# Kernel tuning notes

Hardware: AMD Instinct MI355X
Metric: run time of the kernel (lower is better)

## Reference

```python
import jax, jax.numpy as jnp
import numpy as np
from jax import lax

B, CIN, H, W = 16, 256, 64, 64
DP = 512          # displace_planes
COUT = 256        # outplanes
NUM_OFFSET = 64   # displace_planes // BIND_CHAN(8)
K = 5             # DPOOL_SIZE (odd)
EPS = float(np.finfo(np.float32).eps)
BN_EPS = 1e-5
EXP_CLAMP = 88.722835


def conv1x1(x, w, b):
    # x: [B,C,H,W], w: [O,C], b: [O]
    return jnp.einsum('bchw,oc->bohw', x, w) + b[None, :, None, None]


def batchnorm(x, gamma, beta):
    m = x.mean(axis=(0, 2, 3))
    v = x.var(axis=(0, 2, 3))
    inv = lax.rsqrt(v + BN_EPS)
    return (x - m[None, :, None, None]) * (inv * gamma)[None, :, None, None] + beta[None, :, None, None]


def dynamic_pool(x, sigma):
    # per-channel Gaussian depthwise conv in exp space, back to log space
    r = (jnp.arange(K) - K // 2).astype(jnp.float32)
    dissq = r[:, None] ** 2 + r[None, :] ** 2                     # [K,K]
    kern = jnp.exp(-(dissq / 2.0)[None] / (sigma ** 2 + EPS)[:, None, None])  # [C,K,K]
    kern = kern / kern.sum(axis=(1, 2), keepdims=True)
    expx = jnp.exp(jnp.minimum(x, EXP_CLAMP))
    out = lax.conv_general_dilated(
        expx, kern[:, None],                                      # rhs [C,1,K,K]
        window_strides=(1, 1), padding=[(K // 2, K // 2)] * 2,
        dimension_numbers=('NCHW', 'OIHW', 'NCHW'),
        feature_group_count=DP)
    return jnp.log(out + EPS)


def displace(feat, offsets):
    # feat: [B,C,H,W]; offsets: [NUM_OFFSET,2] (dy,dx), each bound to C//NUM_OFFSET channels.
    # Per-channel uniform bilinear shift with zero padding outside the map.
    Bn, C, Hn, Wn = feat.shape
    chan = C // NUM_OFFSET
    dy = jnp.repeat(offsets[:, 0], chan)  # [C]
    dx = jnp.repeat(offsets[:, 1], chan)
    y0 = jnp.floor(dy); x0 = jnp.floor(dx)
    fy = dy - y0; fx = dx - x0            # fractional parts (diff. wrt offsets)
    y0i = y0.astype(jnp.int32); x0i = x0.astype(jnp.int32)
    rows = jnp.arange(Hn); cols = jnp.arange(Wn)

    def one_chan(img, y0c, x0c, fyc, fxc):
        # img: [B,H,W]; shift is separable per row/col since offset is uniform
        def shifted(oy, ox):
            ry = rows + y0c + oy
            rx = cols + x0c + ox
            my = (ry >= 0) & (ry < Hn)
            mx = (rx >= 0) & (rx < Wn)
            g = img[:, jnp.clip(ry, 0, Hn - 1), :][:, :, jnp.clip(rx, 0, Wn - 1)]
            return g * (my[:, None] & mx[None, :]).astype(img.dtype)[None]
        return ((1 - fyc) * (1 - fxc) * shifted(0, 0)
                + (1 - fyc) * fxc * shifted(0, 1)
                + fyc * (1 - fxc) * shifted(1, 0)
                + fyc * fxc * shifted(1, 1))

    return jax.vmap(one_chan, in_axes=(1, 0, 0, 0, 0), out_axes=1)(feat, y0i, x0i, fy, fx)


def attention(x, w, b, gamma, beta):
    a = conv1x1(x, w, b)
    a = batchnorm(a, gamma, beta)
    a = jax.nn.softplus(a)
    # SpaceNormalization: normalize over spatial dims
    return a / a.sum(axis=(2, 3), keepdims=True)


def setup_inputs() -> dict:
    key = jax.random.key(0)
    ks = jax.random.split(key, 6)
    return {
        'x': jax.random.normal(ks[0], (B, CIN, H, W), jnp.float32),
        'pre_w': jax.random.normal(ks[1], (DP, CIN), jnp.float32) / np.sqrt(CIN),
        'pre_b': jnp.zeros((DP,), jnp.float32),
        'sigma': jnp.full((DP,), K / 2 / 2, jnp.float32),
        'offsets': jax.random.normal(ks[2], (NUM_OFFSET, 2), jnp.float32) * 3.0,
        'atten_w': jax.random.normal(ks[3], (DP, CIN), jnp.float32) / np.sqrt(CIN),
        'atten_b': jnp.zeros((DP,), jnp.float32),
        'atten_gamma': jnp.ones((DP,), jnp.float32),
        'atten_beta': jnp.zeros((DP,), jnp.float32),
        'post_w': jax.random.normal(ks[4], (COUT, DP), jnp.float32) / np.sqrt(DP),
        'post_b': jnp.zeros((COUT,), jnp.float32),
        'bn_gamma': jnp.ones((COUT,), jnp.float32),
        'bn_beta': jnp.zeros((COUT,), jnp.float32),
    }


def reference(x, pre_w, pre_b, sigma, offsets, atten_w, atten_b, atten_gamma,
              atten_beta, post_w, post_b, bn_gamma, bn_beta):
    out_pre = conv1x1(x, pre_w, pre_b)                 # [B,DP,H,W]
    out_pre = dynamic_pool(out_pre, sigma)
    out_dis = displace(out_pre, offsets)
    out_atten = attention(x, atten_w, atten_b, atten_gamma, atten_beta)
    out_post = conv1x1(out_atten * out_dis, post_w, post_b)  # [B,COUT,H,W]
    out_skip = x + out_post                            # inplanes==outplanes, stride=1
    return jax.nn.relu(batchnorm(out_skip, bn_gamma, bn_beta))
```

## Files before the change

kernel.cpp:

```cpp
#include <hip/hip_runtime.h>
#include <cmath>

#define NB   16
#define CINC 256
#define DPC  512
#define COUTC 256
#define HWS  4096
#define EPSF 1.1920928955078125e-07f
#define BN_EPS 1e-5f
#define EXP_CLAMP 88.722835f
#define TS 76
#define PS 72

typedef unsigned int uint32;
typedef unsigned short ushort;
typedef __bf16 bf16x8 __attribute__((ext_vector_type(8)));
typedef float f32x4 __attribute__((ext_vector_type(4)));
typedef unsigned short ushort8 __attribute__((ext_vector_type(8)));

__device__ inline ushort f2bf(float f) {
    __bf16 h = (__bf16)f;
    return __builtin_bit_cast(ushort, h);
}
__device__ inline float bf2f(ushort u) {
    return __builtin_bit_cast(float, (uint32)u << 16);
}
__device__ inline float softplus_fast(float v) {
    return fmaxf(v, 0.f) + __logf(1.f + __expf(-fabsf(v)));
}
__device__ __forceinline__ void gload16(const void* g, void* l) {
    __builtin_amdgcn_global_load_lds(
        (__attribute__((address_space(1))) void*)g,
        (__attribute__((address_space(3))) void*)l, 16, 0, 0);
}

template<int OTOT, int KTOT, bool BF16_OUT, bool ADD_SKIP>
__global__ __launch_bounds__(256) void mfma_gemm_k(
    const ushort* __restrict__ A, const ushort* __restrict__ BT,
    const float* __restrict__ bias1, const float* __restrict__ bias2,
    const float* __restrict__ skip, void* __restrict__ outv) {
    const int hw0 = blockIdx.x * 128;
    const int o0  = blockIdx.y * 128;
    const int b   = blockIdx.z;
    __shared__ ushort As[2 * 128 * 32];
    __shared__ ushort Bs[2 * 128 * 32];
    const int tid  = threadIdx.x;
    const int lane = tid & 63;
    const int w    = tid >> 6;
    const int wm0  = (w >> 1) * 64;
    const int wn0  = (w & 1) * 64;

    f32x4 acc[4][4] = {};

    const ushort* Ab = A + (size_t)o0 * KTOT;
    const ushort* Bb = BT + ((size_t)b * HWS + hw0) * KTOT;
    const int rsub  = lane >> 2;
    const int ksubp = ((lane & 3) ^ ((lane >> 3) & 3)) * 8;

    for (int step = 0; step < KTOT / 64; ++step) {
        const int k0 = step * 64;
#pragma unroll
        for (int h = 0; h < 2; ++h)
#pragma unroll
            for (int i = 0; i < 2; ++i) {
                const int row = w * 32 + i * 16 + rsub;
                gload16(Ab + (size_t)row * KTOT + k0 + h * 32 + ksubp,
                        &As[h * 4096 + (w * 32 + i * 16) * 32]);
                gload16(Bb + (size_t)row * KTOT + k0 + h * 32 + ksubp,
                        &Bs[h * 4096 + (w * 32 + i * 16) * 32]);
            }
        __syncthreads();
        bf16x8 af[2][4], bfr[2][4];
#pragma unroll
        for (int h = 0; h < 2; ++h) {
#pragma unroll
            for (int mi = 0; mi < 4; ++mi) {
                int row = wm0 + mi * 16 + (lane & 15);
                int sl = (lane >> 4) ^ ((row >> 1) & 3);
                af[h][mi] = *reinterpret_cast<const bf16x8*>(As + h * 4096 + row * 32 + sl * 8);
            }
#pragma unroll
            for (int ni = 0; ni < 4; ++ni) {
                int row = wn0 + ni * 16 + (lane & 15);
                int sl = (lane >> 4) ^ ((row >> 1) & 3);
                bfr[h][ni] = *reinterpret_cast<const bf16x8*>(Bs + h * 4096 + row * 32 + sl * 8);
            }
        }
#pragma unroll
        for (int h = 0; h < 2; ++h)
#pragma unroll
            for (int mi = 0; mi < 4; ++mi)
#pragma unroll
                for (int ni = 0; ni < 4; ++ni)
                    acc[mi][ni] = __builtin_amdgcn_mfma_f32_16x16x32_bf16(
                        af[h][mi], bfr[h][ni], acc[mi][ni], 0, 0, 0);
        __syncthreads();
    }

#pragma unroll
    for (int mi = 0; mi < 4; ++mi) {
#pragma unroll
        for (int r = 0; r < 4; ++r) {
            int o = o0 + wm0 + mi * 16 + ((lane >> 4) << 2) + r;
            float bi = (o < 512) ? bias1[o] : bias2[o - 512];
            size_t base = ((size_t)b * OTOT + o) * HWS + hw0 + wn0 + (lane & 15);
            if constexpr (BF16_OUT) {
                ushort* outp = (ushort*)outv;
#pragma unroll
                for (int ni = 0; ni < 4; ++ni)
                    outp[base + ni * 16] = f2bf(acc[mi][ni][r] + bi);
            } else {
                float* outp = (float*)outv;
#pragma unroll
                for (int ni = 0; ni < 4; ++ni) {
                    float v = acc[mi][ni][r] + bi;
                    if constexpr (ADD_SKIP) v += skip[base + ni * 16];
                    outp[base + ni * 16] = v;
                }
            }
        }
    }
}

__global__ __launch_bounds__(256) void castT_k(const float* __restrict__ x,
                                               ushort* __restrict__ xT) {
    const int b = blockIdx.z, c0 = blockIdx.y * 64, hw0 = blockIdx.x * 64;
    __shared__ float tile[64][65];
    const int tid = threadIdx.x;
#pragma unroll
    for (int r = 0; r < 16; ++r) {
        int cl = r * 4 + (tid >> 6), hwl = tid & 63;
        tile[cl][hwl] = x[((size_t)b * CINC + c0 + cl) * HWS + hw0 + hwl];
    }
    __syncthreads();
#pragma unroll
    for (int r = 0; r < 16; ++r) {
        int hwl = r * 4 + (tid >> 6), cl = tid & 63;
        xT[((size_t)b * HWS + hw0 + hwl) * CINC + c0 + cl] = f2bf(tile[cl][hwl]);
    }
}

__global__ __launch_bounds__(256) void cast_k(const float* __restrict__ in,
                                              ushort* __restrict__ out, int n) {
    int i = (blockIdx.x * 256 + threadIdx.x) * 4;
    if (i < n) {
        float4 v = *reinterpret_cast<const float4*>(in + i);
        out[i + 0] = f2bf(v.x); out[i + 1] = f2bf(v.y);
        out[i + 2] = f2bf(v.z); out[i + 3] = f2bf(v.w);
    }
}

__global__ __launch_bounds__(256) void pooldisp_k(ushort* __restrict__ dp,
                                                  const float* __restrict__ sigma,
                                                  const float* __restrict__ offsets) {
    const int bc = blockIdx.x;
    const int b = bc >> 9, c = bc & 511;
    __shared__ float  tmp[68 * TS];
    __shared__ ushort pl[64 * PS];
    const int tid = threadIdx.x;
    ushort* ip = dp + ((size_t)b * 1024 + c) * HWS;

    float s = sigma[c];
    float inv = 0.5f / (s * s + EPSF);
    float g0 = __expf(-4.f * inv), g1 = __expf(-1.f * inv);
    float gs = g0 + g1 + 1.f + g1 + g0;
    float rnorm = 1.f / (gs * gs);

    if (tid < 64) {
        int r = tid >> 4;
        int rr = (r < 2) ? r : 64 + r;
        int cq = (tid & 15) * 4;
        f32x4 z = {0.f, 0.f, 0.f, 0.f};
        *reinterpret_cast<f32x4*>(&tmp[rr * TS + cq]) = z;
    }
#pragma unroll
    for (int t = 0; t < 2; ++t) {
        int task = tid + t * 256;
        int hr = task >> 3, w0 = (task & 7) * 8;
        const ushort* rp = ip + hr * 64 + w0;
        ushort8 mv = *reinterpret_cast<const ushort8*>(rp);
        float e[12];
        e[0] = (w0 > 0) ? __expf(fminf(bf2f(rp[-2]), EXP_CLAMP)) : 0.f;
        e[1] = (w0 > 0) ? __expf(fminf(bf2f(rp[-1]), EXP_CLAMP)) : 0.f;
#pragma unroll
        for (int q = 0; q < 8; ++q)
            e[2 + q] = __expf(fminf(bf2f(mv[q]), EXP_CLAMP));
        e[10] = (w0 < 56) ? __expf(fminf(bf2f(rp[8]), EXP_CLAMP)) : 0.f;
        e[11] = (w0 < 56) ? __expf(fminf(bf2f(rp[9]), EXP_CLAMP)) : 0.f;
        f32x4 o0, o1;
#pragma unroll
        for (int j = 0; j < 4; ++j) {
            o0[j] = g0 * (e[j] + e[j + 4]) + g1 * (e[j + 1] + e[j + 3]) + e[j + 2];
            o1[j] = g0 * (e[j + 4] + e[j + 8]) + g1 * (e[j + 5] + e[j + 7]) + e[j + 6];
        }
        *reinterpret_cast<f32x4*>(&tmp[(hr + 2) * TS + w0]) = o0;
        *reinterpret_cast<f32x4*>(&tmp[(hr + 2) * TS + w0 + 4]) = o1;
    }
    __syncthreads();

#pragma unroll
    for (int t = 0; t < 4; ++t) {
        int task = tid + t * 256;
        int h = task >> 4, wq = (task & 15) * 4;
        f32x4 t0 = *reinterpret_cast<const f32x4*>(&tmp[(h + 0) * TS + wq]);
        f32x4 t1 = *reinterpret_cast<const f32x4*>(&tmp[(h + 1) * TS + wq]);
        f32x4 t2 = *reinterpret_cast<const f32x4*>(&tmp[(h + 2) * TS + wq]);
        f32x4 t3 = *reinterpret_cast<const f32x4*>(&tmp[(h + 3) * TS + wq]);
        f32x4 t4 = *reinterpret_cast<const f32x4*>(&tmp[(h + 4) * TS + wq]);
        ushort o[4];
#pragma unroll
        for (int j = 0; j < 4; ++j) {
            float v = g0 * (t0[j] + t4[j]) + g1 * (t1[j] + t3[j]) + t2[j];
            o[j] = f2bf(__logf(v * rnorm + EPSF));
        }
        *reinterpret_cast<uint32*>(&pl[h * PS + wq]) =
            (uint32)o[0] | ((uint32)o[1] << 16);
        *reinterpret_cast<uint32*>(&pl[h * PS + wq + 2]) =
            (uint32)o[2] | ((uint32)o[3] << 16);
    }
    __syncthreads();

    int oi = c >> 3;
    float dy = offsets[oi * 2 + 0];
    float dx = offsets[oi * 2 + 1];
    float y0f = floorf(dy), x0f = floorf(dx);
    float fy = dy - y0f, fx = dx - x0f;
    int y0 = (int)y0f, x0 = (int)x0f;
    float w00 = (1.f - fy) * (1.f - fx), w01 = (1.f - fy) * fx;
    float w10 = fy * (1.f - fx),         w11 = fy * fx;
#pragma unroll
    for (int t = 0; t < 2; ++t) {
        int p = (tid + t * 256) * 8;
        int h = p >> 6, w = p & 63;
        int ry0 = h + y0, ry1 = ry0 + 1;
        bool my0 = (ry0 >= 0) & (ry0 < 64);
        bool my1 = (ry1 >= 0) & (ry1 < 64);
        ushort8 ov;
#pragma unroll
        for (int q = 0; q < 8; ++q) {
            int rx0 = w + q + x0, rx1 = rx0 + 1;
            bool mx0 = (rx0 >= 0) & (rx0 < 64);
            bool mx1 = (rx1 >= 0) & (rx1 < 64);
            float acc = 0.f;
            if (my0 & mx0) acc += w00 * bf2f(pl[ry0 * PS + rx0]);
            if (my0 & mx1) acc += w01 * bf2f(pl[ry0 * PS + rx1]);
            if (my1 & mx0) acc += w10 * bf2f(pl[ry1 * PS + rx0]);
            if (my1 & mx1) acc += w11 * bf2f(pl[ry1 * PS + rx1]);
            ov[q] = f2bf(acc);
        }
        *reinterpret_cast<ushort8*>(ip + p) = ov;
    }
}

__global__ __launch_bounds__(1024) void attstats_k(const ushort* __restrict__ dp,
                                                   const float* __restrict__ gamma,
                                                   const float* __restrict__ beta,
                                                   float* __restrict__ scale,
                                                   float* __restrict__ shift,
                                                   float* __restrict__ rsum) {
    const int c = blockIdx.x;
    const int t = threadIdx.x;
    const int wv = t >> 6, lane = t & 63;
    const ushort* p = dp + ((size_t)wv * 1024 + 512 + c) * HWS;

    ushort8 v[8];
    float s = 0.f, s2 = 0.f;
#pragma unroll
    for (int k = 0; k < 8; ++k) {
        v[k] = *reinterpret_cast<const ushort8*>(p + lane * 8 + k * 512);
#pragma unroll
        for (int j = 0; j < 8; ++j) { float f = bf2f(v[k][j]); s += f; s2 += f * f; }
    }
#pragma unroll
    for (int off = 32; off > 0; off >>= 1) {
        s += __shfl_down(s, off, 64);
        s2 += __shfl_down(s2, off, 64);
    }
    __shared__ float t1[16], t2[16], scsh[2];
    if (lane == 0) { t1[wv] = s; t2[wv] = s2; }
    __syncthreads();
    if (t == 0) {
        float S = 0.f, S2 = 0.f;
#pragma unroll
        for (int k = 0; k < 16; ++k) { S += t1[k]; S2 += t2[k]; }
        float n = (float)(NB * HWS);
        float mean = S / n;
        float var = S2 / n - mean * mean;
        float invs = rsqrtf(var + BN_EPS);
        float sc = invs * gamma[c];
        float sh = beta[c] - mean * sc;
        scale[c] = sc; shift[c] = sh;
        scsh[0] = sc; scsh[1] = sh;
    }
    __syncthreads();
    float sc = scsh[0], sh = scsh[1];
    float ps = 0.f;
#pragma unroll
    for (int k = 0; k < 8; ++k)
#pragma unroll
        for (int j = 0; j < 8; ++j)
            ps += softplus_fast(bf2f(v[k][j]) * sc + sh);
#pragma unroll
    for (int off = 32; off > 0; off >>= 1) ps += __shfl_down(ps, off, 64);
    if (lane == 0) rsum[wv * DPC + c] = 1.f / ps;
}

__global__ __launch_bounds__(256) void attmulT_k(const ushort* __restrict__ dp,
                                                 const float* __restrict__ scale,
                                                 const float* __restrict__ shift,
                                                 const float* __restrict__ rsum,
                                                 ushort* __restrict__ mT) {
    const int b = blockIdx.z, c0 = blockIdx.y * 64, hw0 = blockIdx.x * 64;
    __shared__ float tile[64][65];
    const int tid = threadIdx.x;
#pragma unroll
    for (int r = 0; r < 16; ++r) {
        int cl = r * 4 + (tid >> 6), hwl = tid & 63;
        int c = c0 + cl;
        size_t aidx = ((size_t)b * 1024 + 512 + c) * HWS + hw0 + hwl;
        size_t didx = ((size_t)b * 1024 + c) * HWS + hw0 + hwl;
        float a = bf2f(dp[aidx]) * scale[c] + shift[c];
        float m = softplus_fast(a) * rsum[b * DPC + c] * bf2f(dp[didx]);
        tile[cl][hwl] = m;
    }
    __syncthreads();
#pragma unroll
    for (int r = 0; r < 16; ++r) {
        int hwl = r * 4 + (tid >> 6), cl = tid & 63;
        mT[((size_t)b * HWS + hw0 + hwl) * DPC + c0 + cl] = f2bf(tile[cl][hwl]);
    }
}

__global__ __launch_bounds__(1024) void bnstats_k(const float* __restrict__ a,
                                                  const float* __restrict__ gamma,
                                                  const float* __restrict__ beta,
                                                  float* __restrict__ scale,
                                                  float* __restrict__ shift) {
    const int c = blockIdx.x;
    const int t = threadIdx.x;
    const int wv = t >> 6, lane = t & 63;
    const float* p = a + ((size_t)wv * COUTC + c) * HWS;
    float s = 0.f, s2 = 0.f;
#pragma unroll
    for (int k = 0; k < 16; ++k) {
        float4 v = *reinterpret_cast<const float4*>(p + lane * 4 + k * 256);
        s += v.x + v.y + v.z + v.w;
        s2 += v.x * v.x + v.y * v.y + v.z * v.z + v.w * v.w;
    }
#pragma unroll
    for (int off = 32; off > 0; off >>= 1) {
        s += __shfl_down(s, off, 64);
        s2 += __shfl_down(s2, off, 64);
    }
    __shared__ float t1[16], t2[16];
    if (lane == 0) { t1[wv] = s; t2[wv] = s2; }
    __syncthreads();
    if (t == 0) {
        float S = 0.f, S2 = 0.f;
#pragma unroll
        for (int k = 0; k < 16; ++k) { S += t1[k]; S2 += t2[k]; }
        float n = (float)(NB * HWS);
        float mean = S / n;
        float var = S2 / n - mean * mean;
        float invs = rsqrtf(var + BN_EPS);
        float sc = invs * gamma[c];
        scale[c] = sc;
        shift[c] = beta[c] - mean * sc;
    }
}

__global__ __launch_bounds__(256) void final_k(float* __restrict__ out,
                                               const float* __restrict__ scale,
                                               const float* __restrict__ shift) {
    int i = blockIdx.x * 256 + threadIdx.x;
    int c = (i >> 12) & (COUTC - 1);
    float v = out[i] * scale[c] + shift[c];
    out[i] = fmaxf(v, 0.f);
}

extern "C" void kernel_launch(void* const* d_in, const int* in_sizes, int n_in,
                              void* d_out, int out_size, void* d_ws, size_t ws_size,
                              hipStream_t stream) {
    const float* x           = (const float*)d_in[0];
    const float* pre_w       = (const float*)d_in[1];
    const float* pre_b       = (const float*)d_in[2];
    const float* sigma       = (const float*)d_in[3];
    const float* offsets     = (const float*)d_in[4];
    const float* atten_w     = (const float*)d_in[5];
    const float* atten_b     = (const float*)d_in[6];
    const float* atten_gamma = (const float*)d_in[7];
    const float* atten_beta  = (const float*)d_in[8];
    const float* post_w      = (const float*)d_in[9];
    const float* post_b      = (const float*)d_in[10];
    const float* bn_gamma    = (const float*)d_in[11];
    const float* bn_beta     = (const float*)d_in[12];
    float* out = (float*)d_out;

    char* wsb = (char*)d_ws;
    ushort* xT    = (ushort*)(wsb);
    ushort* wbig  = (ushort*)(wsb + ((size_t)32 << 20));
    ushort* wpost = wbig + 1024 * 256;
    float*  stats = (float*)(wsb + ((size_t)33 << 20));
    ushort* dpout = (ushort*)(wsb + ((size_t)34 << 20));
    ushort* mT    = (ushort*)(wsb + ((size_t)162 << 20));

    float* scaleA = stats;
    float* shiftA = stats + 512;
    float* rsum   = stats + 1024;
    float* scale2 = stats + 9216;
    float* shift2 = stats + 9472;

    castT_k<<<dim3(64, 4, NB), 256, 0, stream>>>(x, xT);
    cast_k<<<128, 256, 0, stream>>>(pre_w,   wbig,             DPC * CINC);
    cast_k<<<128, 256, 0, stream>>>(atten_w, wbig + 512 * 256, DPC * CINC);
    cast_k<<<128, 256, 0, stream>>>(post_w,  wpost,            COUTC * DPC);

    mfma_gemm_k<1024, CINC, true, false><<<dim3(32, 8, NB), 256, 0, stream>>>(
        wbig, xT, pre_b, atten_b, nullptr, dpout);
    pooldisp_k<<<NB * DPC, 256, 0, stream>>>(dpout, sigma, offsets);
    attstats_k<<<DPC, 1024, 0, stream>>>(dpout, atten_gamma, atten_beta,
                                         scaleA, shiftA, rsum);
    attmulT_k<<<dim3(64, 8, NB), 256, 0, stream>>>(dpout, scaleA, shiftA, rsum, mT);
    mfma_gemm_k<COUTC, DPC, false, true><<<dim3(32, 2, NB), 256, 0, stream>>>(
        wpost, mT, post_b, post_b, x, out);
    bnstats_k<<<COUTC, 1024, 0, stream>>>(out, bn_gamma, bn_beta, scale2, shift2);
    final_k<<<out_size / 256, 256, 0, stream>>>(out, scale2, shift2);
}
```

Baseline: 297.9 us.

## Widen pool/displace blocks to 512 threads and reuse shifted row samples

The fused pool+displace kernel now runs with 512 threads per block and one task per thread instead of looping, with launch bounds asking for higher occupancy. The bilinear displacement loads 9 samples per row once into registers and reuses them across the 8 outputs, replacing 32 guarded LDS reads with 18. The plane LDS stride is changed to 66 to alter bank mapping. This may raise register pressure under the tighter launch bounds.

```diff
diff --git a/kernel.cpp b/kernel.cpp
--- a/kernel.cpp
+++ b/kernel.cpp
@@ -10,7 +10,7 @@
 #define BN_EPS 1e-5f
 #define EXP_CLAMP 88.722835f
 #define TS 76
-#define PS 72
+#define PS2 66
 
 typedef unsigned int uint32;
 typedef unsigned short ushort;
@@ -150,13 +150,13 @@
     }
 }
 
-__global__ __launch_bounds__(256) void pooldisp_k(ushort* __restrict__ dp,
-                                                  const float* __restrict__ sigma,
-                                                  const float* __restrict__ offsets) {
+__global__ __launch_bounds__(512, 8) void pooldisp_k(ushort* __restrict__ dp,
+                                                     const float* __restrict__ sigma,
+                                                     const float* __restrict__ offsets) {
     const int bc = blockIdx.x;
     const int b = bc >> 9, c = bc & 511;
     __shared__ float  tmp[68 * TS];
-    __shared__ ushort pl[64 * PS];
+    __shared__ ushort pl[64 * PS2];
     const int tid = threadIdx.x;
     ushort* ip = dp + ((size_t)b * 1024 + c) * HWS;
 
@@ -166,17 +166,15 @@
     float gs = g0 + g1 + 1.f + g1 + g0;
     float rnorm = 1.f / (gs * gs);
 
-    if (tid < 64) {
-        int r = tid >> 4;
-        int rr = (r < 2) ? r : 64 + r;
-        int cq = (tid & 15) * 4;
-        f32x4 z = {0.f, 0.f, 0.f, 0.f};
-        *reinterpret_cast<f32x4*>(&tmp[rr * TS + cq]) = z;
-    }
-#pragma unroll
-    for (int t = 0; t < 2; ++t) {
-        int task = tid + t * 256;
-        int hr = task >> 3, w0 = (task & 7) * 8;
+    {
+        int r4 = tid >> 7, col = tid & 127;
+        if (col < TS) {
+            int row = (r4 < 2) ? r4 : 64 + r4;
+            tmp[row * TS + col] = 0.f;
+        }
+    }
+    {
+        int hr = tid >> 3, w0 = (tid & 7) * 8;
         const ushort* rp = ip + hr * 64 + w0;
         ushort8 mv = *reinterpret_cast<const ushort8*>(rp);
         float e[12];
@@ -199,8 +197,8 @@
     __syncthreads();
 
 #pragma unroll
-    for (int t = 0; t < 4; ++t) {
-        int task = tid + t * 256;
+    for (int t = 0; t < 2; ++t) {
+        int task = tid + t * 512;
         int h = task >> 4, wq = (task & 15) * 4;
         f32x4 t0 = *reinterpret_cast<const f32x4*>(&tmp[(h + 0) * TS + wq]);
         f32x4 t1 = *reinterpret_cast<const f32x4*>(&tmp[(h + 1) * TS + wq]);
@@ -213,42 +211,40 @@
             float v = g0 * (t0[j] + t4[j]) + g1 * (t1[j] + t3[j]) + t2[j];
             o[j] = f2bf(__logf(v * rnorm + EPSF));
         }
-        *reinterpret_cast<uint32*>(&pl[h * PS + wq]) =
+        *reinterpret_cast<uint32*>(&pl[h * PS2 + wq]) =
             (uint32)o[0] | ((uint32)o[1] << 16);
-        *reinterpret_cast<uint32*>(&pl[h * PS + wq + 2]) =
+        *reinterpret_cast<uint32*>(&pl[h * PS2 + wq + 2]) =
             (uint32)o[2] | ((uint32)o[3] << 16);
     }
     __syncthreads();
 
-    int oi = c >> 3;
-    float dy = offsets[oi * 2 + 0];
-    float dx = offsets[oi * 2 + 1];
-    float y0f = floorf(dy), x0f = floorf(dx);
-    float fy = dy - y0f, fx = dx - x0f;
-    int y0 = (int)y0f, x0 = (int)x0f;
-    float w00 = (1.f - fy) * (1.f - fx), w01 = (1.f - fy) * fx;
-    float w10 = fy * (1.f - fx),         w11 = fy * fx;
-#pragma unroll
-    for (int t = 0; t < 2; ++t) {
-        int p = (tid + t * 256) * 8;
-        int h = p >> 6, w = p & 63;
+    {
+        int oi = c >> 3;
+        float dy = offsets[oi * 2 + 0];
+        float dx = offsets[oi * 2 + 1];
+        float y0f = floorf(dy), x0f = floorf(dx);
+        float fy = dy - y0f, fx = dx - x0f;
+        int y0 = (int)y0f, x0 = (int)x0f;
+        float w00 = (1.f - fy) * (1.f - fx), w01 = (1.f - fy) * fx;
+        float w10 = fy * (1.f - fx),         w11 = fy * fx;
+        int h = tid >> 3, w = (tid & 7) * 8;
         int ry0 = h + y0, ry1 = ry0 + 1;
         bool my0 = (ry0 >= 0) & (ry0 < 64);
         bool my1 = (ry1 >= 0) & (ry1 < 64);
+        float e0[9], e1[9];
+#pragma unroll
+        for (int j = 0; j < 9; ++j) {
+            int col = w + x0 + j;
+            bool mx = (col >= 0) & (col < 64);
+            e0[j] = (my0 & mx) ? bf2f(pl[ry0 * PS2 + col]) : 0.f;
+            e1[j] = (my1 & mx) ? bf2f(pl[ry1 * PS2 + col]) : 0.f;
+        }
         ushort8 ov;
 #pragma unroll
-        for (int q = 0; q < 8; ++q) {
-            int rx0 = w + q + x0, rx1 = rx0 + 1;
-            bool mx0 = (rx0 >= 0) & (rx0 < 64);
-            bool mx1 = (rx1 >= 0) & (rx1 < 64);
-            float acc = 0.f;
-            if (my0 & mx0) acc += w00 * bf2f(pl[ry0 * PS + rx0]);
-            if (my0 & mx1) acc += w01 * bf2f(pl[ry0 * PS + rx1]);
-            if (my1 & mx0) acc += w10 * bf2f(pl[ry1 * PS + rx0]);
-            if (my1 & mx1) acc += w11 * bf2f(pl[ry1 * PS + rx1]);
-            ov[q] = f2bf(acc);
-        }
-        *reinterpret_cast<ushort8*>(ip + p) = ov;
+        for (int q = 0; q < 8; ++q)
+            ov[q] = f2bf(w00 * e0[q] + w01 * e0[q + 1]
+                       + w10 * e1[q] + w11 * e1[q + 1]);
+        *reinterpret_cast<ushort8*>(ip + tid * 8) = ov;
     }
 }
 
@@ -417,7 +413,7 @@
 
     mfma_gemm_k<1024, CINC, true, false><<<dim3(32, 8, NB), 256, 0, stream>>>(
         wbig, xT, pre_b, atten_b, nullptr, dpout);
-    pooldisp_k<<<NB * DPC, 256, 0, stream>>>(dpout, sigma, offsets);
+    pooldisp_k<<<NB * DPC, 512, 0, stream>>>(dpout, sigma, offsets);
     attstats_k<<<DPC, 1024, 0, stream>>>(dpout, atten_gamma, atten_beta,
                                          scaleA, shiftA, rsum);
     attmulT_k<<<dim3(64, 8, NB), 256, 0, stream>>>(dpout, scaleA, shiftA, rsum, mT);
```

After: 288.1 us. 3.3% less time.
